# Optimization experiments

Hardware: AMD Instinct MI355X
Metric: run time of the kernel (lower is better)

## Reference

```python
import jax, jax.numpy as jnp
import numpy as np


def setup_inputs() -> dict:
    key = jax.random.key(0)
    k1, k2 = jax.random.split(key)
    L = 1_000_000  # 1000x1000 meshgrid, flattened
    B = 256        # number of receiver positions
    mesh_2D = jax.random.uniform(k1, (L, 2), dtype=jnp.float32) * 10.0  # room coords in [0,10)m
    receiver_pos = jax.random.uniform(k2, (B, 3), dtype=jnp.float32) * 10.0
    return {"mesh_2D": mesh_2D, "receiver_pos": receiver_pos}


def reference(mesh_2D, receiver_pos):
    # mesh_2D: [L, 2], receiver_pos: [B, 3]
    X = mesh_2D[:, 0]  # [L]
    Y = mesh_2D[:, 1]  # [L]
    # Brute-force receiver-to-mesh squared distances, [B, L].
    # (sqrt is monotone, so argmin over squared distances == argmin over distances)
    d2 = (X[None, :] - receiver_pos[:, 0:1]) ** 2 + (Y[None, :] - receiver_pos[:, 1:2]) ** 2
    min_index = jnp.argmin(d2, axis=1).astype(jnp.int32)  # [B]
    L = X.shape[0]
    one_hot = jnp.zeros((L, 1), dtype=mesh_2D.dtype)
    one_hot = one_hot.at[min_index, 0].set(1.0)
    # Faithful to the torch loop quirk: at iteration k<B-1 the not-yet-filled
    # entries of min_index are 0, so index 0 is also set to 1 whenever B > 1.
    if receiver_pos.shape[0] > 1:
        one_hot = one_hot.at[0, 0].set(1.0)
    closest_points = jnp.stack([X[min_index], Y[min_index]], axis=1)  # [B, 2]
    input_tensor = jnp.concatenate([X[:, None], Y[:, None], one_hot], axis=1).astype(jnp.float32)  # [L, 3]
    return input_tensor, closest_points, min_index
```

## Files before the change

kernel.cpp:

```cpp
#include <hip/hip_runtime.h>
#include <math.h>


#define G      256
#define GG     (G * G)
#define BMW    (GG / 32)
#define CELLW  (10.0f / (float)G)
#define W2     (CELLW * CELLW)
#define INVW   ((float)G / 10.0f)
#define CAP    64
#define PBASE  ((int)0xAAAAAAAA)
#define NCHUNK 1024

__device__ __forceinline__ int clampi(int v, int lo, int hi) {
    return min(max(v, lo), hi);
}

__device__ __forceinline__ int cell_of(float x, float y) {
    int cx = clampi((int)(x * INVW), 0, G - 1);
    int cy = clampi((int)(y * INVW), 0, G - 1);
    return cy * G + cx;
}


__global__ void filter_copy_kernel(const float4* __restrict__ mesh4,
                                   float4* __restrict__ out4,
                                   const float* __restrict__ recv,
                                   int* __restrict__ cellcnt,
                                   float4* __restrict__ cellbuf,
                                   int L, int B) {
    __shared__ unsigned sbm[BMW];
    int tt = threadIdx.x;
    for (int i = tt; i < BMW; i += 256) sbm[i] = 0u;
    __syncthreads();
    for (int r = tt; r < B; r += 256) {
        float rx = recv[3 * r + 0];
        float ry = recv[3 * r + 1];
        int cx = clampi((int)(rx * INVW), 0, G - 1);
        int cy = clampi((int)(ry * INVW), 0, G - 1);
        for (int uy = max(cy - 1, 0); uy <= min(cy + 1, G - 1); ++uy)
            for (int ux = max(cx - 1, 0); ux <= min(cx + 1, G - 1); ++ux) {
                int c = uy * G + ux;
                atomicOr(&sbm[c >> 5], 1u << (c & 31));
            }
    }
    __syncthreads();

    const int nt4 = (L + 3) / 4;
    const int stride = gridDim.x * blockDim.x;
    for (int t = blockIdx.x * blockDim.x + tt; t < nt4; t += stride) {
        int p0 = t * 4;

        float xs[4], ys[4];
        if (p0 + 3 < L) {
            float4 a = mesh4[2 * t];
            float4 b = mesh4[2 * t + 1];
            out4[3 * t + 0] = make_float4(a.x, a.y, 0.0f, a.z);
            out4[3 * t + 1] = make_float4(a.w, 0.0f, b.x, b.y);
            out4[3 * t + 2] = make_float4(0.0f, b.z, b.w, 0.0f);
            xs[0] = a.x; ys[0] = a.y; xs[1] = a.z; ys[1] = a.w;
            xs[2] = b.x; ys[2] = b.y; xs[3] = b.z; ys[3] = b.w;
        } else {
            const float2* mesh = (const float2*)mesh4;
            float* out0 = (float*)out4;
            for (int k = 0; k < 4; ++k) {
                int p = p0 + k;
                if (p >= L) { xs[k] = -100.0f; ys[k] = -100.0f; continue; }
                float2 pt = mesh[p];
                out0[3 * (size_t)p + 0] = pt.x;
                out0[3 * (size_t)p + 1] = pt.y;
                out0[3 * (size_t)p + 2] = 0.0f;
                xs[k] = pt.x; ys[k] = pt.y;
            }
        }

        int c[4];
        unsigned w[4];
        #pragma unroll
        for (int k = 0; k < 4; ++k) c[k] = cell_of(xs[k], ys[k]);
        #pragma unroll
        for (int k = 0; k < 4; ++k) w[k] = sbm[c[k] >> 5];

        #pragma unroll
        for (int k = 0; k < 4; ++k) {
            int p = p0 + k;
            if (p >= L) continue;
            if ((w[k] >> (c[k] & 31)) & 1u) {
                int slot = atomicAdd(&cellcnt[c[k]], 1) - PBASE;
                if (slot >= 0 && slot < CAP) {
                    cellbuf[(size_t)c[k] * CAP + slot] =
                        make_float4(xs[k], ys[k], __int_as_float(p), 0.0f);
                }
            }
        }
    }
}

__global__ void argmin_final_kernel(const float2* __restrict__ mesh,
                                    const float* __restrict__ recv,
                                    const int* __restrict__ cellcnt,
                                    const float4* __restrict__ cellbuf,
                                    float* __restrict__ out0,
                                    float* __restrict__ out1,
                                    float* __restrict__ out2,
                                    int L, int B) {
    int wid = (blockIdx.x * blockDim.x + threadIdx.x) >> 6;
    int lane = threadIdx.x & 63;
    if (wid >= B) return;

    float rx = recv[3 * wid + 0];
    float ry = recv[3 * wid + 1];
    int cx = clampi((int)(rx * INVW), 0, G - 1);
    int cy = clampi((int)(ry * INVW), 0, G - 1);

    float bd2 = INFINITY;
    int bidx = 0x7fffffff;
    bool overflow = false;

    for (int uy = max(cy - 1, 0); uy <= min(cy + 1, G - 1); ++uy) {
        for (int ux = max(cx - 1, 0); ux <= min(cx + 1, G - 1); ++ux) {
            int c = uy * G + ux;
            int n = cellcnt[c] - PBASE;
            if (n < 0 || n > CAP) { overflow = true; n = clampi(n, 0, CAP); }
            size_t base = (size_t)c * CAP;
            for (int j = lane; j < n; j += 64) {
                float4 e = cellbuf[base + j];
                int pi = __float_as_int(e.z);
                float dx = e.x - rx;
                float dy = e.y - ry;
                float d2 = __fadd_rn(__fmul_rn(dx, dx), __fmul_rn(dy, dy));
                if (d2 < bd2 || (d2 == bd2 && pi < bidx)) { bd2 = d2; bidx = pi; }
            }
        }
    }

    float rb = bd2;
    int ri = bidx;
    for (int m = 1; m < 64; m <<= 1) {
        float ob = __shfl_xor(rb, m, 64);
        int   oi = __shfl_xor(ri, m, 64);
        if (ob < rb || (ob == rb && oi < ri)) { rb = ob; ri = oi; }
    }

    bool ok = !overflow && (rb < 0.98f * W2);
    if (!ok) {
        bd2 = INFINITY; bidx = 0x7fffffff;
        for (int j = lane; j < L; j += 64) {
            float2 p = mesh[j];
            float dx = p.x - rx;
            float dy = p.y - ry;
            float d2 = __fadd_rn(__fmul_rn(dx, dx), __fmul_rn(dy, dy));
            if (d2 < bd2 || (d2 == bd2 && j < bidx)) { bd2 = d2; bidx = j; }
        }
        rb = bd2; ri = bidx;
        for (int m = 1; m < 64; m <<= 1) {
            float ob = __shfl_xor(rb, m, 64);
            int   oi = __shfl_xor(ri, m, 64);
            if (ob < rb || (ob == rb && oi < ri)) { rb = ob; ri = oi; }
        }
    }

    if (lane == 0) {
        out2[wid] = (float)ri;
        float2 p = mesh[ri];
        out1[2 * wid + 0] = p.x;
        out1[2 * wid + 1] = p.y;
        out0[3 * (size_t)ri + 2] = 1.0f;
        if (wid == 0 && B > 1) out0[2] = 1.0f;
    }
}


__global__ void copy_xy_kernel(const float2* __restrict__ mesh,
                               float* __restrict__ out0, int L) {
    int i = blockIdx.x * blockDim.x + threadIdx.x;
    if (i < L) {
        float2 p = mesh[i];
        out0[3 * i + 0] = p.x;
        out0[3 * i + 1] = p.y;
        out0[3 * i + 2] = 0.0f;
    }
}

__global__ void partial_argmin_kernel(const float2* __restrict__ mesh,
                                      const float* __restrict__ recv,
                                      float* __restrict__ pd2,
                                      int* __restrict__ pidx,
                                      int L, int chunk) {
    const int b = threadIdx.x;
    const int c = blockIdx.x;
    const float rx = recv[3 * b + 0];
    const float ry = recv[3 * b + 1];
    int start = c * chunk;
    int end = min(start + chunk, L);

    float best = INFINITY;
    int bidx = 0x7fffffff;
    #pragma unroll 8
    for (int l = start; l < end; ++l) {
        float2 p = mesh[l];
        float dx = p.x - rx;
        float dy = p.y - ry;
        float d2 = __fadd_rn(__fmul_rn(dx, dx), __fmul_rn(dy, dy));
        if (d2 < best) { best = d2; bidx = l; }
    }
    pd2[c * blockDim.x + b] = best;
    pidx[c * blockDim.x + b] = bidx;
}

__global__ void reduce_finalize_kernel(const float2* __restrict__ mesh,
                                       const float* __restrict__ pd2,
                                       const int* __restrict__ pidx,
                                       float* __restrict__ out0,
                                       float* __restrict__ out1,
                                       float* __restrict__ out2,
                                       int B) {
    const int b = blockIdx.x;
    const int t = threadIdx.x;

    float best = INFINITY;
    int bidx = 0x7fffffff;
    for (int c = t; c < NCHUNK; c += blockDim.x) {
        float d2 = pd2[c * B + b];
        int   i  = pidx[c * B + b];
        if (d2 < best || (d2 == best && i < bidx)) { best = d2; bidx = i; }
    }

    __shared__ float sd[256];
    __shared__ int   si[256];
    sd[t] = best;
    si[t] = bidx;
    __syncthreads();
    for (int s = 128; s > 0; s >>= 1) {
        if (t < s) {
            float d2 = sd[t + s];
            int   i  = si[t + s];
            if (d2 < sd[t] || (d2 == sd[t] && i < si[t])) { sd[t] = d2; si[t] = i; }
        }
        __syncthreads();
    }

    if (t == 0) {
        int idx = si[0];
        out2[b] = (float)idx;
        float2 p = mesh[idx];
        out1[2 * b + 0] = p.x;
        out1[2 * b + 1] = p.y;
        out0[3 * (size_t)idx + 2] = 1.0f;
        if (b == 0) out0[2] = 1.0f;
    }
}

extern "C" void kernel_launch(void* const* d_in, const int* in_sizes, int n_in,
                              void* d_out, int out_size, void* d_ws, size_t ws_size,
                              hipStream_t stream) {
    const float* mesh = (const float*)d_in[0];
    const float* recv = (const float*)d_in[1];
    const int L = in_sizes[0] / 2;
    const int B = in_sizes[1] / 3;

    float* out0 = (float*)d_out;
    float* out1 = out0 + (size_t)3 * L;
    float* out2 = out1 + (size_t)2 * B;

    const size_t need = (size_t)GG * sizeof(int)
                      + (size_t)GG * CAP * sizeof(float4);

    if (ws_size >= need && B <= 4096) {
        int* cellcnt    = (int*)d_ws;
        float4* cellbuf = (float4*)((char*)d_ws + (size_t)GG * sizeof(int));

        filter_copy_kernel<<<512, 256, 0, stream>>>(
            (const float4*)mesh, (float4*)out0, recv, cellcnt, cellbuf, L, B);
        argmin_final_kernel<<<(B * 64 + 255) / 256, 256, 0, stream>>>(
            (const float2*)mesh, recv, cellcnt, cellbuf,
            out0, out1, out2, L, B);
    } else {
        float* pd2  = (float*)d_ws;
        int*   pidx = (int*)((char*)d_ws + sizeof(float) * (size_t)NCHUNK * B);
        const int chunk = (L + NCHUNK - 1) / NCHUNK;

        copy_xy_kernel<<<(L + 255) / 256, 256, 0, stream>>>(
            (const float2*)mesh, out0, L);
        partial_argmin_kernel<<<NCHUNK, B, 0, stream>>>(
            (const float2*)mesh, recv, pd2, pidx, L, chunk);
        reduce_finalize_kernel<<<B, 256, 0, stream>>>(
            (const float2*)mesh, pd2, pidx, out0, out1, out2, B);
    }
}
```

Baseline: 76.19 us.

## Process each receiver with a full block over flattened 3x3 cell list

Replaces the one-wavefront-per-receiver argmin with one 256-thread block per receiver. The nine neighbouring cell counts are prefix-summed in shared memory so all candidate points are spread across the block, followed by a shared-memory tree reduction. The aim is to cut the serial per-cell loops and raise parallelism in the small final kernel. In exchange it adds several __syncthreads barriers, and the brute-force fallback now runs with 256 threads.

```diff
diff --git a/kernel.cpp b/kernel.cpp
--- a/kernel.cpp
+++ b/kernel.cpp
@@ -7,6 +7,7 @@
 #define BMW    (GG / 32)
 #define CELLW  (10.0f / (float)G)
 #define W2     (CELLW * CELLW)
+#define GATE   (0.98f * W2)
 #define INVW   ((float)G / 10.0f)
 #define CAP    64
 #define PBASE  ((int)0xAAAAAAAA)
@@ -96,7 +97,7 @@
     }
 }
 
-__global__ void argmin_final_kernel(const float2* __restrict__ mesh,
+__global__ void argmin_block_kernel(const float2* __restrict__ mesh,
                                     const float* __restrict__ recv,
                                     const int* __restrict__ cellcnt,
                                     const float4* __restrict__ cellbuf,
@@ -104,69 +105,101 @@
                                     float* __restrict__ out1,
                                     float* __restrict__ out2,
                                     int L, int B) {
-    int wid = (blockIdx.x * blockDim.x + threadIdx.x) >> 6;
-    int lane = threadIdx.x & 63;
-    if (wid >= B) return;
-
-    float rx = recv[3 * wid + 0];
-    float ry = recv[3 * wid + 1];
+    const int r = blockIdx.x;
+    const int t = threadIdx.x;
+    if (r >= B) return;
+
+    __shared__ int scell[9];
+    __shared__ int scnt[9];
+    __shared__ int sbase[10];
+    __shared__ int soflow;
+    __shared__ float sd[256];
+    __shared__ int   si[256];
+
+    float rx = recv[3 * r + 0];
+    float ry = recv[3 * r + 1];
     int cx = clampi((int)(rx * INVW), 0, G - 1);
     int cy = clampi((int)(ry * INVW), 0, G - 1);
 
+    if (t == 0) soflow = 0;
+    __syncthreads();
+    if (t < 9) {
+        int ux = cx + (t % 3) - 1;
+        int uy = cy + (t / 3) - 1;
+        int cell = -1, n = 0;
+        if (ux >= 0 && ux < G && uy >= 0 && uy < G) {
+            cell = uy * G + ux;
+            n = cellcnt[cell] - PBASE;
+            if (n < 0 || n > CAP) { atomicOr(&soflow, 1); n = clampi(n, 0, CAP); }
+        }
+        scell[t] = cell;
+        scnt[t] = n;
+    }
+    __syncthreads();
+    if (t == 0) {
+        int acc = 0;
+        for (int i = 0; i < 9; ++i) { sbase[i] = acc; acc += scnt[i]; }
+        sbase[9] = acc;
+    }
+    __syncthreads();
+
+    int total = sbase[9];
     float bd2 = INFINITY;
     int bidx = 0x7fffffff;
-    bool overflow = false;
-
-    for (int uy = max(cy - 1, 0); uy <= min(cy + 1, G - 1); ++uy) {
-        for (int ux = max(cx - 1, 0); ux <= min(cx + 1, G - 1); ++ux) {
-            int c = uy * G + ux;
-            int n = cellcnt[c] - PBASE;
-            if (n < 0 || n > CAP) { overflow = true; n = clampi(n, 0, CAP); }
-            size_t base = (size_t)c * CAP;
-            for (int j = lane; j < n; j += 64) {
-                float4 e = cellbuf[base + j];
-                int pi = __float_as_int(e.z);
-                float dx = e.x - rx;
-                float dy = e.y - ry;
-                float d2 = __fadd_rn(__fmul_rn(dx, dx), __fmul_rn(dy, dy));
-                if (d2 < bd2 || (d2 == bd2 && pi < bidx)) { bd2 = d2; bidx = pi; }
-            }
-        }
-    }
-
-    float rb = bd2;
-    int ri = bidx;
-    for (int m = 1; m < 64; m <<= 1) {
-        float ob = __shfl_xor(rb, m, 64);
-        int   oi = __shfl_xor(ri, m, 64);
-        if (ob < rb || (ob == rb && oi < ri)) { rb = ob; ri = oi; }
-    }
-
-    bool ok = !overflow && (rb < 0.98f * W2);
+    for (int pos = t; pos < total; pos += 256) {
+        int ci = 0;
+        while (pos >= sbase[ci + 1]) ++ci;
+        float4 e = cellbuf[(size_t)scell[ci] * CAP + (pos - sbase[ci])];
+        int pi = __float_as_int(e.z);
+        float dx = e.x - rx;
+        float dy = e.y - ry;
+        float d2 = __fadd_rn(__fmul_rn(dx, dx), __fmul_rn(dy, dy));
+        if (d2 < bd2 || (d2 == bd2 && pi < bidx)) { bd2 = d2; bidx = pi; }
+    }
+    sd[t] = bd2;
+    si[t] = bidx;
+    __syncthreads();
+    for (int s = 128; s > 0; s >>= 1) {
+        if (t < s) {
+            float d2 = sd[t + s];
+            int   i  = si[t + s];
+            if (d2 < sd[t] || (d2 == sd[t] && i < si[t])) { sd[t] = d2; si[t] = i; }
+        }
+        __syncthreads();
+    }
+
+    bool ok = (soflow == 0) && (sd[0] < GATE) && (si[0] >= 0) && (si[0] < L);
     if (!ok) {
         bd2 = INFINITY; bidx = 0x7fffffff;
-        for (int j = lane; j < L; j += 64) {
+        for (int j = t; j < L; j += 256) {
             float2 p = mesh[j];
             float dx = p.x - rx;
             float dy = p.y - ry;
             float d2 = __fadd_rn(__fmul_rn(dx, dx), __fmul_rn(dy, dy));
             if (d2 < bd2 || (d2 == bd2 && j < bidx)) { bd2 = d2; bidx = j; }
         }
-        rb = bd2; ri = bidx;
-        for (int m = 1; m < 64; m <<= 1) {
-            float ob = __shfl_xor(rb, m, 64);
-            int   oi = __shfl_xor(ri, m, 64);
-            if (ob < rb || (ob == rb && oi < ri)) { rb = ob; ri = oi; }
-        }
-    }
-
-    if (lane == 0) {
-        out2[wid] = (float)ri;
-        float2 p = mesh[ri];
-        out1[2 * wid + 0] = p.x;
-        out1[2 * wid + 1] = p.y;
-        out0[3 * (size_t)ri + 2] = 1.0f;
-        if (wid == 0 && B > 1) out0[2] = 1.0f;
+        __syncthreads();
+        sd[t] = bd2;
+        si[t] = bidx;
+        __syncthreads();
+        for (int s = 128; s > 0; s >>= 1) {
+            if (t < s) {
+                float d2 = sd[t + s];
+                int   i  = si[t + s];
+                if (d2 < sd[t] || (d2 == sd[t] && i < si[t])) { sd[t] = d2; si[t] = i; }
+            }
+            __syncthreads();
+        }
+    }
+
+    if (t == 0) {
+        int idx = si[0];
+        out2[r] = (float)idx;
+        float2 p = mesh[idx];
+        out1[2 * r + 0] = p.x;
+        out1[2 * r + 1] = p.y;
+        out0[3 * (size_t)idx + 2] = 1.0f;
+        if (r == 0 && B > 1) out0[2] = 1.0f;
     }
 }
 
@@ -272,7 +305,7 @@
 
         filter_copy_kernel<<<512, 256, 0, stream>>>(
             (const float4*)mesh, (float4*)out0, recv, cellcnt, cellbuf, L, B);
-        argmin_final_kernel<<<(B * 64 + 255) / 256, 256, 0, stream>>>(
+        argmin_block_kernel<<<B, 256, 0, stream>>>(
             (const float2*)mesh, recv, cellcnt, cellbuf,
             out0, out1, out2, L, B);
     } else {
```

After: 71.28 us (median of 3 runs). 6.4% less time.
